# Kernel tuning notes

Measured on AMD Instinct MI355X. Metric: run time of the kernel, lower is better.

The kernel has to match this reference:

```python
import jax, jax.numpy as jnp
import numpy as np

B, S1, S2 = 8, 2048, 2048
K1D = K2D = V1D = V2D = 256
A = 128


def setup_inputs() -> dict:
    key = jax.random.key(0)
    ks = jax.random.split(key, 8)
    k1 = jax.random.normal(ks[0], (B, S1, K1D), dtype=jnp.float32)
    k2 = jax.random.normal(ks[1], (B, S2, K2D), dtype=jnp.float32)
    v1 = jax.random.normal(ks[2], (B, S1, V1D), dtype=jnp.float32)
    v2 = jax.random.normal(ks[3], (B, S2, V2D), dtype=jnp.float32)
    Wk1 = jax.random.normal(ks[4], (K1D, A), dtype=jnp.float32) / np.sqrt(K1D)
    Wk2 = jax.random.normal(ks[5], (K2D, A), dtype=jnp.float32) / np.sqrt(K2D)
    bk1 = jnp.zeros((A,), dtype=jnp.float32)
    bk2 = jnp.zeros((A,), dtype=jnp.float32)
    # lengths in [1, S-1]: avoids fully-masked softmax rows (NaN) under the XOR mask
    k1_lengths = jax.random.randint(ks[6], (B,), 1, S1, dtype=jnp.int64)
    k2_lengths = jax.random.randint(ks[7], (B,), 1, S2, dtype=jnp.int64)
    return {"k1": k1, "k2": k2, "v1": v1, "v2": v2,
            "Wk1": Wk1, "bk1": bk1, "Wk2": Wk2, "bk2": bk2,
            "k1_lengths": k1_lengths, "k2_lengths": k2_lengths}


def reference(k1, k2, v1, v2, Wk1, bk1, Wk2, bk2, k1_lengths, k2_lengths):
    b, s1, _ = k1.shape
    s2 = k2.shape[1]
    mask1 = jnp.arange(s1)[None, :] < k1_lengths[:, None]  # [B,S1] bool
    mask2 = jnp.arange(s2)[None, :] < k2_lengths[:, None]  # [B,S2] bool
    # masked where exactly one side is valid (sum == 1)
    amask = (mask1[:, :, None].astype(jnp.int32)
             + mask2[:, None, :].astype(jnp.int32)) == 1  # [B,S1,S2]
    p1 = k1 @ Wk1 + bk1  # [B,S1,A]
    p2 = k2 @ Wk2 + bk2  # [B,S2,A]
    score = jnp.einsum('bia,bja->bij', p1, p2)  # [B,S1,S2]
    score = jnp.where(amask, -jnp.inf, score)
    w1 = jax.nn.softmax(score.transpose(0, 2, 1), axis=-1)  # [B,S2,S1]
    w2 = jax.nn.softmax(score, axis=-1)                      # [B,S1,S2]
    o1 = jnp.einsum('bji,bid->bjd', w1, v1) * mask2[:, :, None].astype(v1.dtype)  # [B,S2,V1D]
    o2 = jnp.einsum('bij,bjd->bid', w2, v2) * mask1[:, :, None].astype(v2.dtype)  # [B,S1,V2D]
    return (o1, o2, w1, w2, score)
```

## Files before the change

kernel.cpp:

```cpp
#include <hip/hip_runtime.h>
#include <cstddef>

#define NB 8
#define SEQ 2048
#define KD 256
#define AD 128
#define VD 256

#define NEG_BIG (-3.0e38f)

typedef __attribute__((ext_vector_type(8))) short short8v;
typedef __attribute__((ext_vector_type(4))) float f32x4;

static __device__ __forceinline__ unsigned f2o(float f) {
    unsigned u = __float_as_uint(f);
    return (u & 0x80000000u) ? ~u : (u | 0x80000000u);
}
static __device__ __forceinline__ float o2f(unsigned o) {
    unsigned u = (o & 0x80000000u) ? (o ^ 0x80000000u) : ~o;
    return __uint_as_float(u);
}

static __device__ __forceinline__ unsigned packsplit(float w) {
    unsigned u = __float_as_uint(w);
    unsigned h = (u + 0x7fffu + ((u >> 16) & 1u)) >> 16;
    float hf = __uint_as_float(h << 16);
    unsigned u2 = __float_as_uint(w - hf);
    unsigned l = (u2 + 0x7fffu + ((u2 >> 16) & 1u)) >> 16;
    return (h << 16) | l;
}

static __device__ __forceinline__ unsigned packtrunc(float x) {
    unsigned u = __float_as_uint(x);
    unsigned hi = u & 0xffff0000u;
    float lof = x - __uint_as_float(hi);
    return hi | (__float_as_uint(lof) >> 16);
}

static __device__ __forceinline__ void unpack_frag(const unsigned* rowp, int c0,
                                                   short8v& hi, short8v& lo) {
    uint4 a = *(const uint4*)(rowp + c0);
    uint4 b = *(const uint4*)(rowp + ((c0 + 4) & 31));
    hi[0] = (short)(a.x >> 16); lo[0] = (short)(a.x);
    hi[1] = (short)(a.y >> 16); lo[1] = (short)(a.y);
    hi[2] = (short)(a.z >> 16); lo[2] = (short)(a.z);
    hi[3] = (short)(a.w >> 16); lo[3] = (short)(a.w);
    hi[4] = (short)(b.x >> 16); lo[4] = (short)(b.x);
    hi[5] = (short)(b.y >> 16); lo[5] = (short)(b.y);
    hi[6] = (short)(b.z >> 16); lo[6] = (short)(b.z);
    hi[7] = (short)(b.w >> 16); lo[7] = (short)(b.w);
}

__global__ __launch_bounds__(64) void init_kernel(
        const int* __restrict__ l1raw, const int* __restrict__ l2raw,
        int* __restrict__ lens) {
    if (threadIdx.x == 0 && blockIdx.x == 0) {
        bool i64a = (l1raw[1] == 0 && l1raw[3] == 0 && l1raw[5] == 0 && l1raw[7] == 0);
        bool i64b = (l2raw[1] == 0 && l2raw[3] == 0 && l2raw[5] == 0 && l2raw[7] == 0);
        for (int i = 0; i < NB; ++i) {
            lens[i]      = i64a ? l1raw[2 * i] : l1raw[i];
            lens[NB + i] = i64b ? l2raw[2 * i] : l2raw[i];
        }
    }
}

__global__ __launch_bounds__(256) void proj_kernel(
        const float* __restrict__ X, const float* __restrict__ W,
        const float* __restrict__ bias, float* __restrict__ P) {
    const int m0 = blockIdx.x * 64;
    const int tx = threadIdx.x % 16, ty = threadIdx.x / 16;
    __shared__ float Xs[32][68];
    __shared__ float Ws[32][132];
    float acc[4][8] = {};
    for (int k0 = 0; k0 < KD; k0 += 32) {
        {
            int t = threadIdx.x;
            int m = t >> 2;
            int fbase = (t & 3) * 2;
            const float4* src = (const float4*)(X + (size_t)(m0 + m) * KD + k0);
            #pragma unroll
            for (int q = 0; q < 2; ++q) {
                float4 v = src[fbase + q];
                int k = (fbase + q) * 4;
                Xs[k + 0][m] = v.x; Xs[k + 1][m] = v.y;
                Xs[k + 2][m] = v.z; Xs[k + 3][m] = v.w;
            }
        }
        {
            int t = threadIdx.x;
            int k = t >> 3;
            int fb = (t & 7) * 4;
            const float4* src = (const float4*)(W + (size_t)(k0 + k) * AD);
            float4* dst = (float4*)(&Ws[k][0]);
            #pragma unroll
            for (int q = 0; q < 4; ++q) dst[fb + q] = src[fb + q];
        }
        __syncthreads();
        #pragma unroll 8
        for (int kk = 0; kk < 32; ++kk) {
            float4 a = ((const float4*)(&Xs[kk][0]))[ty];
            float4 b0 = ((const float4*)(&Ws[kk][0]))[tx];
            float4 b1 = ((const float4*)(&Ws[kk][0]))[tx + 16];
            float av[4] = {a.x, a.y, a.z, a.w};
            float bv[8] = {b0.x, b0.y, b0.z, b0.w, b1.x, b1.y, b1.z, b1.w};
            #pragma unroll
            for (int i = 0; i < 4; ++i)
                #pragma unroll
                for (int j = 0; j < 8; ++j)
                    acc[i][j] = fmaf(av[i], bv[j], acc[i][j]);
        }
        __syncthreads();
    }
    float4 bias0 = ((const float4*)bias)[tx];
    float4 bias1 = ((const float4*)bias)[tx + 16];
    #pragma unroll
    for (int i = 0; i < 4; ++i) {
        int m = m0 + 4 * ty + i;
        float4 r0 = make_float4(acc[i][0] + bias0.x, acc[i][1] + bias0.y,
                                acc[i][2] + bias0.z, acc[i][3] + bias0.w);
        float4 r1 = make_float4(acc[i][4] + bias1.x, acc[i][5] + bias1.y,
                                acc[i][6] + bias1.z, acc[i][7] + bias1.w);
        float4* dst = (float4*)(P + (size_t)m * AD);
        dst[tx] = r0;
        dst[tx + 16] = r1;
    }
}

__global__ __launch_bounds__(256) void score_kernel(
        const float* __restrict__ P1, const float* __restrict__ P2,
        const int* __restrict__ lens, float* __restrict__ score,
        float* __restrict__ rp_max, float* __restrict__ rp_sum,
        float* __restrict__ cp_max, float* __restrict__ cp_sum) {
    const int b = blockIdx.z;
    const int i0 = blockIdx.y * 128, j0 = blockIdx.x * 128;
    const int tx = threadIdx.x % 16, ty = threadIdx.x / 16;
    __shared__ float As[32][132];
    __shared__ float Bs[32][132];
    __shared__ unsigned rmax_l[128], cmax_l[128];
    __shared__ float rsum_l[128], csum_l[128];
    float acc[8][8] = {};
    for (int a0 = 0; a0 < AD; a0 += 32) {
        int t = threadIdx.x;
        int r = t >> 1;
        int fb = (t & 1) * 4;
        const float4* s1 = (const float4*)(P1 + (size_t)(b * SEQ + i0 + r) * AD + a0);
        const float4* s2 = (const float4*)(P2 + (size_t)(b * SEQ + j0 + r) * AD + a0);
        #pragma unroll
        for (int q = 0; q < 4; ++q) {
            float4 v = s1[fb + q];
            float4 w = s2[fb + q];
            int k = (fb + q) * 4;
            As[k + 0][r] = v.x; As[k + 1][r] = v.y; As[k + 2][r] = v.z; As[k + 3][r] = v.w;
            Bs[k + 0][r] = w.x; Bs[k + 1][r] = w.y; Bs[k + 2][r] = w.z; Bs[k + 3][r] = w.w;
        }
        __syncthreads();
        #pragma unroll 4
        for (int kk = 0; kk < 32; ++kk) {
            const float4* Ar = (const float4*)(&As[kk][0]);
            const float4* Br = (const float4*)(&Bs[kk][0]);
            float4 a0v = Ar[ty], a1v = Ar[ty + 16];
            float4 b0v = Br[tx], b1v = Br[tx + 16];
            float av[8] = {a0v.x, a0v.y, a0v.z, a0v.w, a1v.x, a1v.y, a1v.z, a1v.w};
            float bv[8] = {b0v.x, b0v.y, b0v.z, b0v.w, b1v.x, b1v.y, b1v.z, b1v.w};
            #pragma unroll
            for (int i = 0; i < 8; ++i)
                #pragma unroll
                for (int j = 0; j < 8; ++j)
                    acc[i][j] = fmaf(av[i], bv[j], acc[i][j]);
        }
        __syncthreads();
    }
    const int len1 = lens[b], len2 = lens[NB + b];
    if (threadIdx.x < 128) {
        rmax_l[threadIdx.x] = 0u; cmax_l[threadIdx.x] = 0u; csum_l[threadIdx.x] = 0.f;
    }
    __syncthreads();
    unsigned cpart[8] = {0u, 0u, 0u, 0u, 0u, 0u, 0u, 0u};
    #pragma unroll
    for (int ii = 0; ii < 8; ++ii) {
        int il = 4 * ty + (ii & 3) + ((ii >> 2) << 6);
        int ig = i0 + il;
        bool va = ig < len1;
        unsigned rpart = 0u;
        float vals[8];
        #pragma unroll
        for (int jj = 0; jj < 8; ++jj) {
            int jl = 4 * tx + (jj & 3) + ((jj >> 2) << 6);
            int jg = j0 + jl;
            bool vb = jg < len2;
            float s = (va != vb) ? NEG_BIG : acc[ii][jj];
            vals[jj] = s;
            unsigned o = f2o(s);
            rpart = rpart > o ? rpart : o;
            cpart[jj] = cpart[jj] > o ? cpart[jj] : o;
        }
        float* dst = score + (size_t)(b * SEQ + ig) * SEQ + j0;
        ((float4*)dst)[tx]      = make_float4(vals[0], vals[1], vals[2], vals[3]);
        ((float4*)dst)[tx + 16] = make_float4(vals[4], vals[5], vals[6], vals[7]);
        atomicMax(&rmax_l[il], rpart);
    }
    #pragma unroll
    for (int jj = 0; jj < 8; ++jj) {
        int jl = 4 * tx + (jj & 3) + ((jj >> 2) << 6);
        atomicMax(&cmax_l[jl], cpart[jj]);
    }
    __syncthreads();
    float cmaxv[8];
    #pragma unroll
    for (int jj = 0; jj < 8; ++jj) {
        int jl = 4 * tx + (jj & 3) + ((jj >> 2) << 6);
        cmaxv[jj] = o2f(cmax_l[jl]);
    }
    float cs[8] = {};
    #pragma unroll
    for (int ii = 0; ii < 8; ++ii) {
        int il = 4 * ty + (ii & 3) + ((ii >> 2) << 6);
        int ig = i0 + il;
        bool va = ig < len1;
        float rmx = o2f(rmax_l[il]);
        float rs = 0.f;
        #pragma unroll
        for (int jj = 0; jj < 8; ++jj) {
            int jl = 4 * tx + (jj & 3) + ((jj >> 2) << 6);
            bool vb = (j0 + jl) < len2;
            float s = (va != vb) ? NEG_BIG : acc[ii][jj];
            rs += __expf(s - rmx);
            cs[jj] += __expf(s - cmaxv[jj]);
        }
        rs += __shfl_xor(rs, 1); rs += __shfl_xor(rs, 2);
        rs += __shfl_xor(rs, 4); rs += __shfl_xor(rs, 8);
        if (tx == 0) rsum_l[il] = rs;
    }
    #pragma unroll
    for (int jj = 0; jj < 8; ++jj) {
        float v = cs[jj];
        v += __shfl_xor(v, 16); v += __shfl_xor(v, 32);
        if (((threadIdx.x >> 4) & 3) == 0) {
            int jl = 4 * tx + (jj & 3) + ((jj >> 2) << 6);
            atomicAdd(&csum_l[jl], v);
        }
    }
    __syncthreads();
    if (threadIdx.x < 128) {
        int tt = threadIdx.x;
        size_t ri = (size_t)(b * 16 + blockIdx.x) * SEQ + i0 + tt;
        size_t ci = (size_t)(b * 16 + blockIdx.y) * SEQ + j0 + tt;
        rp_max[ri] = o2f(rmax_l[tt]);
        rp_sum[ri] = rsum_l[tt];
        cp_max[ci] = o2f(cmax_l[tt]);
        cp_sum[ci] = csum_l[tt];
    }
}

__global__ __launch_bounds__(256) void combine_kernel(
        const float* __restrict__ rp_max, const float* __restrict__ rp_sum,
        const float* __restrict__ cp_max, const float* __restrict__ cp_sum,
        float* __restrict__ rowmaxf, float* __restrict__ rowinv,
        float* __restrict__ colmaxf, float* __restrict__ colinv) {
    int gid = blockIdx.x * 256 + threadIdx.x;
    bool isCol = gid >= NB * SEQ;
    int r = isCol ? gid - NB * SEQ : gid;
    int bb = r >> 11, pos = r & (SEQ - 1);
    const float* pm = (isCol ? cp_max : rp_max) + ((size_t)(bb * 16) << 11) + pos;
    const float* ps = (isCol ? cp_sum : rp_sum) + ((size_t)(bb * 16) << 11) + pos;
    float m = pm[0];
    #pragma unroll
    for (int t = 1; t < 16; ++t) m = fmaxf(m, pm[(size_t)t << 11]);
    float s = 0.f;
    #pragma unroll
    for (int t = 0; t < 16; ++t)
        s += ps[(size_t)t << 11] * __expf(pm[(size_t)t << 11] - m);
    if (isCol) { colmaxf[r] = m; colinv[r] = 1.f / s; }
    else       { rowmaxf[r] = m; rowinv[r] = 1.f / s; }
}

__global__ __launch_bounds__(256) void o2_mfma_kernel(
        const float* __restrict__ score, const float* __restrict__ rmaxf,
        const float* __restrict__ rinvv, const float* __restrict__ V2,
        const int* __restrict__ lens, float* __restrict__ w2,
        float* __restrict__ o2) {
    const int b = blockIdx.y;
    const int m0 = blockIdx.x * 32;
    const int t = threadIdx.x;
    const int wid = t >> 6, lane = t & 63;
    const int wr = wid >> 1, wc = wid & 1;
    const int l15 = lane & 15, l4 = lane >> 4;

    __shared__ unsigned Au[32][32];
    __shared__ unsigned Bu[256][32];

    const int ia = t >> 3;
    const int jf4 = (t & 7) * 4;
    const float arm = rmaxf[b * SEQ + m0 + ia];
    const float ari = rinvv[b * SEQ + m0 + ia];
    const float* srow = score + (size_t)(b * SEQ + m0 + ia) * SEQ;
    float* wrow = w2 + (size_t)(b * SEQ + m0 + ia) * SEQ;

    const int kb = t >> 3;
    const int df = t & 7;
    const float* vbase = V2 + (size_t)(b * SEQ + kb) * VD + df * 4;

    f32x4 accM[8] = {};
    f32x4 accC[8] = {};

    float4 sc;
    float4 vv[8];
    sc = *(const float4*)(srow + jf4);
    #pragma unroll
    for (int c = 0; c < 2; ++c)
        #pragma unroll
        for (int q = 0; q < 4; ++q)
            vv[c * 4 + q] = *(const float4*)(vbase + c * 128 + q * 32);

    for (int k0 = 0; k0 < SEQ; k0 += 32) {
        float wv0 = __expf(sc.x - arm) * ari;
        float wv1 = __expf(sc.y - arm) * ari;
        float wv2 = __expf(sc.z - arm) * ari;
        float wv3 = __expf(sc.w - arm) * ari;
        uint4 pa;
        pa.x = packsplit(wv0); pa.y = packsplit(wv1);
        pa.z = packsplit(wv2); pa.w = packsplit(wv3);
        __syncthreads();
        *(uint4*)&Au[ia][(jf4 + 4 * (ia & 7)) & 31] = pa;
        #pragma unroll
        for (int c = 0; c < 2; ++c)
            #pragma unroll
            for (int q = 0; q < 4; ++q) {
                float4 v = vv[c * 4 + q];
                int d0 = c * 128 + q * 32 + df * 4;
                Bu[d0 + 0][(kb + 4 * (((d0 + 0) + ((d0 + 0) >> 4)) & 7)) & 31] = packtrunc(v.x);
                Bu[d0 + 1][(kb + 4 * (((d0 + 1) + ((d0 + 1) >> 4)) & 7)) & 31] = packtrunc(v.y);
                Bu[d0 + 2][(kb + 4 * (((d0 + 2) + ((d0 + 2) >> 4)) & 7)) & 31] = packtrunc(v.z);
                Bu[d0 + 3][(kb + 4 * (((d0 + 3) + ((d0 + 3) >> 4)) & 7)) & 31] = packtrunc(v.w);
            }
        __syncthreads();
        if (k0 + 32 < SEQ) {
            sc = *(const float4*)(srow + k0 + 32 + jf4);
            const float* vr = vbase + (size_t)(k0 + 32) * VD;
            #pragma unroll
            for (int c = 0; c < 2; ++c)
                #pragma unroll
                for (int q = 0; q < 4; ++q)
                    vv[c * 4 + q] = *(const float4*)(vr + c * 128 + q * 32);
        }
        *(float4*)(wrow + k0 + jf4) = make_float4(wv0, wv1, wv2, wv3);
        short8v ahi, alo;
        {
            int row = wr * 16 + l15;
            unpack_frag(&Au[row][0], (8 * l4 + 4 * (row & 7)) & 31, ahi, alo);
        }
        #pragma unroll
        for (int fj = 0; fj < 8; ++fj) {
            int d = wc * 128 + fj * 16 + l15;
            int c0 = (8 * l4 + 4 * ((d + (d >> 4)) & 7)) & 31;
            short8v bhi, blo;
            unpack_frag(&Bu[d][0], c0, bhi, blo);
            accM[fj] = __builtin_amdgcn_mfma_f32_16x16x32_bf16(ahi, bhi, accM[fj], 0, 0, 0);
            accC[fj] = __builtin_amdgcn_mfma_f32_16x16x32_bf16(ahi, blo, accC[fj], 0, 0, 0);
            accC[fj] = __builtin_amdgcn_mfma_f32_16x16x32_bf16(alo, bhi, accC[fj], 0, 0, 0);
        }
    }
    const int len1 = lens[b];
    #pragma unroll
    for (int r = 0; r < 4; ++r) {
        int m = m0 + wr * 16 + l4 * 4 + r;
        bool valid = m < len1;
        float* orow = o2 + (size_t)(b * SEQ + m) * VD + wc * 128 + l15;
        #pragma unroll
        for (int fj = 0; fj < 8; ++fj)
            orow[fj * 16] = valid ? (accM[fj][r] + accC[fj][r]) : 0.f;
    }
}

__global__ __launch_bounds__(256) void o1_mfma_kernel(
        const float* __restrict__ score, const float* __restrict__ cmaxf,
        const float* __restrict__ cinvv, const float* __restrict__ V1,
        const int* __restrict__ lens, float* __restrict__ w1,
        float* __restrict__ o1) {
    const int b = blockIdx.y;
    const int m0 = blockIdx.x * 32;
    const int t = threadIdx.x;
    const int wid = t >> 6, lane = t & 63;
    const int wr = wid >> 1, wc = wid & 1;
    const int l15 = lane & 15, l4 = lane >> 4;

    __shared__ unsigned Au[32][32];
    __shared__ unsigned Bu[256][32];

    const int il = t >> 3;
    const int jf4 = (t & 7) * 4;
    float4 cm = *(const float4*)(cmaxf + b * SEQ + m0 + jf4);
    float4 ci = *(const float4*)(cinvv + b * SEQ + m0 + jf4);
    const float* scol = score + (size_t)(b * SEQ + il) * SEQ + m0 + jf4;

    const int kb = t >> 3;
    const int df = t & 7;
    const float* vbase = V1 + (size_t)(b * SEQ + kb) * VD + df * 4;

    const int wj = t >> 3;
    const int wib = (t & 7) * 4;
    const int rc0 = (wib + 4 * (wj & 7)) & 31;
    float* w1row = w1 + (size_t)(b * SEQ + m0 + wj) * SEQ;

    f32x4 accM[8] = {};
    f32x4 accC[8] = {};

    float4 sc;
    float4 vv[8];
    sc = *(const float4*)(scol);
    #pragma unroll
    for (int c = 0; c < 2; ++c)
        #pragma unroll
        for (int q = 0; q < 4; ++q)
            vv[c * 4 + q] = *(const float4*)(vbase + c * 128 + q * 32);

    for (int k0 = 0; k0 < SEQ; k0 += 32) {
        float wvv[4];
        wvv[0] = __expf(sc.x - cm.x) * ci.x;
        wvv[1] = __expf(sc.y - cm.y) * ci.y;
        wvv[2] = __expf(sc.z - cm.z) * ci.z;
        wvv[3] = __expf(sc.w - cm.w) * ci.w;
        unsigned pk[4];
        #pragma unroll
        for (int e = 0; e < 4; ++e) pk[e] = packsplit(wvv[e]);
        __syncthreads();
        #pragma unroll
        for (int e = 0; e < 4; ++e)
            Au[jf4 + e][(il + 4 * ((jf4 + e) & 7)) & 31] = pk[e];
        #pragma unroll
        for (int c = 0; c < 2; ++c)
            #pragma unroll
            for (int q = 0; q < 4; ++q) {
                float4 v = vv[c * 4 + q];
                int d0 = c * 128 + q * 32 + df * 4;
                Bu[d0 + 0][(kb + 4 * (((d0 + 0) + ((d0 + 0) >> 4)) & 7)) & 31] = packtrunc(v.x);
                Bu[d0 + 1][(kb + 4 * (((d0 + 1) + ((d0 + 1) >> 4)) & 7)) & 31] = packtrunc(v.y);
                Bu[d0 + 2][(kb + 4 * (((d0 + 2) + ((d0 + 2) >> 4)) & 7)) & 31] = packtrunc(v.z);
                Bu[d0 + 3][(kb + 4 * (((d0 + 3) + ((d0 + 3) >> 4)) & 7)) & 31] = packtrunc(v.w);
            }
        __syncthreads();
        if (k0 + 32 < SEQ) {
            sc = *(const float4*)(scol + (size_t)(k0 + 32) * SEQ);
            const float* vr = vbase + (size_t)(k0 + 32) * VD;
            #pragma unroll
            for (int c = 0; c < 2; ++c)
                #pragma unroll
                for (int q = 0; q < 4; ++q)
                    vv[c * 4 + q] = *(const float4*)(vr + c * 128 + q * 32);
        }
        {
            uint4 a = *(const uint4*)(&Au[wj][rc0]);
            float f0 = __uint_as_float(a.x & 0xffff0000u) + __uint_as_float(a.x << 16);
            float f1 = __uint_as_float(a.y & 0xffff0000u) + __uint_as_float(a.y << 16);
            float f2 = __uint_as_float(a.z & 0xffff0000u) + __uint_as_float(a.z << 16);
            float f3 = __uint_as_float(a.w & 0xffff0000u) + __uint_as_float(a.w << 16);
            *(float4*)(w1row + k0 + wib) = make_float4(f0, f1, f2, f3);
        }
        short8v ahi, alo;
        {
            int row = wr * 16 + l15;
            unpack_frag(&Au[row][0], (8 * l4 + 4 * (row & 7)) & 31, ahi, alo);
        }
        #pragma unroll
        for (int fj = 0; fj < 8; ++fj) {
            int d = wc * 128 + fj * 16 + l15;
            int c0 = (8 * l4 + 4 * ((d + (d >> 4)) & 7)) & 31;
            short8v bhi, blo;
            unpack_frag(&Bu[d][0], c0, bhi, blo);
            accM[fj] = __builtin_amdgcn_mfma_f32_16x16x32_bf16(ahi, bhi, accM[fj], 0, 0, 0);
            accC[fj] = __builtin_amdgcn_mfma_f32_16x16x32_bf16(ahi, blo, accC[fj], 0, 0, 0);
            accC[fj] = __builtin_amdgcn_mfma_f32_16x16x32_bf16(alo, bhi, accC[fj], 0, 0, 0);
        }
    }
    const int len2 = lens[NB + b];
    #pragma unroll
    for (int r = 0; r < 4; ++r) {
        int m = m0 + wr * 16 + l4 * 4 + r;
        bool valid = m < len2;
        float* orow = o1 + (size_t)(b * SEQ + m) * VD + wc * 128 + l15;
        #pragma unroll
        for (int fj = 0; fj < 8; ++fj)
            orow[fj * 16] = valid ? (accM[fj][r] + accC[fj][r]) : 0.f;
    }
}

extern "C" void kernel_launch(void* const* d_in, const int* in_sizes, int n_in,
                              void* d_out, int out_size, void* d_ws, size_t ws_size,
                              hipStream_t stream) {
    const float* k1  = (const float*)d_in[0];
    const float* k2  = (const float*)d_in[1];
    const float* v1  = (const float*)d_in[2];
    const float* v2  = (const float*)d_in[3];
    const float* Wk1 = (const float*)d_in[4];
    const float* bk1 = (const float*)d_in[5];
    const float* Wk2 = (const float*)d_in[6];
    const float* bk2 = (const float*)d_in[7];
    const int* l1raw = (const int*)d_in[8];
    const int* l2raw = (const int*)d_in[9];

    float* out = (float*)d_out;
    float* o1    = out;
    float* o2    = o1 + (size_t)NB * SEQ * VD;
    float* w1    = o2 + (size_t)NB * SEQ * VD;
    float* w2    = w1 + (size_t)NB * SEQ * SEQ;
    float* score = w2 + (size_t)NB * SEQ * SEQ;

    char* ws = (char*)d_ws;
    float* p1 = (float*)ws;
    float* p2 = p1 + (size_t)NB * SEQ * AD;
    float* rowmaxf = p2 + (size_t)NB * SEQ * AD;
    float* rowinv  = rowmaxf + NB * SEQ;
    float* colmaxf = rowinv + NB * SEQ;
    float* colinv  = colmaxf + NB * SEQ;
    int* lens = (int*)(colinv + NB * SEQ);

    const size_t PTS = (size_t)NB * 16 * SEQ;
    float* rp_max = w1;
    float* rp_sum = w1 + PTS;
    float* cp_max = w1 + 2 * PTS;
    float* cp_sum = w1 + 3 * PTS;

    init_kernel<<<1, 64, 0, stream>>>(l1raw, l2raw, lens);
    proj_kernel<<<256, 256, 0, stream>>>(k1, Wk1, bk1, p1);
    proj_kernel<<<256, 256, 0, stream>>>(k2, Wk2, bk2, p2);
    score_kernel<<<dim3(16, 16, NB), 256, 0, stream>>>(p1, p2, lens, score,
                                                       rp_max, rp_sum, cp_max, cp_sum);
    combine_kernel<<<128, 256, 0, stream>>>(rp_max, rp_sum, cp_max, cp_sum,
                                            rowmaxf, rowinv, colmaxf, colinv);
    o2_mfma_kernel<<<dim3(64, NB), 256, 0, stream>>>(score, rowmaxf, rowinv,
                                                     v2, lens, w2, o2);
    o1_mfma_kernel<<<dim3(64, NB), 256, 0, stream>>>(score, colmaxf, colinv,
                                                     v1, lens, w1, o1);
}
```

Before: 841.4 us.

## Pre-pack V into split-bf16 MFMA-ready blobs and retile output per wave

New measurement: 1.337 ms. 58.9% more time.

```diff
diff --git a/kernel.cpp b/kernel.cpp
--- a/kernel.cpp
+++ b/kernel.cpp
@@ -28,13 +28,6 @@
     unsigned u2 = __float_as_uint(w - hf);
     unsigned l = (u2 + 0x7fffu + ((u2 >> 16) & 1u)) >> 16;
     return (h << 16) | l;
-}
-
-static __device__ __forceinline__ unsigned packtrunc(float x) {
-    unsigned u = __float_as_uint(x);
-    unsigned hi = u & 0xffff0000u;
-    float lof = x - __uint_as_float(hi);
-    return hi | (__float_as_uint(lof) >> 16);
 }
 
 static __device__ __forceinline__ void unpack_frag(const unsigned* rowp, int c0,
@@ -274,45 +267,66 @@
     else       { rowmaxf[r] = m; rowinv[r] = 1.f / s; }
 }
 
+__global__ __launch_bounds__(256) void vpack_kernel(
+        const float* __restrict__ V, unsigned* __restrict__ Vp) {
+    const int b = blockIdx.y, kt = blockIdx.x;
+    const int d = threadIdx.x;
+    const float* src = V + ((size_t)(b * SEQ) + kt * 32) * VD + d;
+    unsigned h[32], l[32];
+    #pragma unroll
+    for (int kk = 0; kk < 32; ++kk) {
+        float x = src[(size_t)kk * VD];
+        unsigned u = __float_as_uint(x);
+        unsigned hh = (u + 0x7fffu + ((u >> 16) & 1u)) >> 16;
+        float hf = __uint_as_float(hh << 16);
+        unsigned u2 = __float_as_uint(x - hf);
+        unsigned ll = (u2 + 0x7fffu + ((u2 >> 16) & 1u)) >> 16;
+        h[kk] = hh; l[kk] = ll;
+    }
+    unsigned* blob = Vp + (size_t)(b * 64 + kt) * 8192;
+    #pragma unroll
+    for (int c = 0; c < 4; ++c) {
+        int kbase = 8 * ((c - (d >> 1)) & 3);
+        uint4 hv, lv;
+        hv.x = h[kbase + 0] | (h[kbase + 1] << 16); hv.y = h[kbase + 2] | (h[kbase + 3] << 16);
+        hv.z = h[kbase + 4] | (h[kbase + 5] << 16); hv.w = h[kbase + 6] | (h[kbase + 7] << 16);
+        lv.x = l[kbase + 0] | (l[kbase + 1] << 16); lv.y = l[kbase + 2] | (l[kbase + 3] << 16);
+        lv.z = l[kbase + 4] | (l[kbase + 5] << 16); lv.w = l[kbase + 6] | (l[kbase + 7] << 16);
+        *(uint4*)(blob + d * 16 + c * 4)        = hv;
+        *(uint4*)(blob + 4096 + d * 16 + c * 4) = lv;
+    }
+}
+
 __global__ __launch_bounds__(256) void o2_mfma_kernel(
         const float* __restrict__ score, const float* __restrict__ rmaxf,
-        const float* __restrict__ rinvv, const float* __restrict__ V2,
+        const float* __restrict__ rinvv, const unsigned* __restrict__ Vp,
         const int* __restrict__ lens, float* __restrict__ w2,
         float* __restrict__ o2) {
     const int b = blockIdx.y;
     const int m0 = blockIdx.x * 32;
     const int t = threadIdx.x;
     const int wid = t >> 6, lane = t & 63;
-    const int wr = wid >> 1, wc = wid & 1;
     const int l15 = lane & 15, l4 = lane >> 4;
 
     __shared__ unsigned Au[32][32];
-    __shared__ unsigned Bu[256][32];
-
-    const int ia = t >> 3;
-    const int jf4 = (t & 7) * 4;
+    __shared__ __align__(16) unsigned Bs[8192];
+
+    const int ia = t >> 3, jf4 = (t & 7) * 4;
     const float arm = rmaxf[b * SEQ + m0 + ia];
     const float ari = rinvv[b * SEQ + m0 + ia];
     const float* srow = score + (size_t)(b * SEQ + m0 + ia) * SEQ;
     float* wrow = w2 + (size_t)(b * SEQ + m0 + ia) * SEQ;
 
-    const int kb = t >> 3;
-    const int df = t & 7;
-    const float* vbase = V2 + (size_t)(b * SEQ + kb) * VD + df * 4;
-
-    f32x4 accM[8] = {};
-    f32x4 accC[8] = {};
-
-    float4 sc;
-    float4 vv[8];
-    sc = *(const float4*)(srow + jf4);
-    #pragma unroll
-    for (int c = 0; c < 2; ++c)
-        #pragma unroll
-        for (int q = 0; q < 4; ++q)
-            vv[c * 4 + q] = *(const float4*)(vbase + c * 128 + q * 32);
-
-    for (int k0 = 0; k0 < SEQ; k0 += 32) {
+    const unsigned* vpb = Vp + (size_t)b * (64 * 8192) + wid * 2048 + lane * 4;
+
+    f32x4 accM[2][4] = {}, accC[2][4] = {};
+    float4 sc = *(const float4*)(srow + jf4);
+    uint4 bvv[8];
+    #pragma unroll
+    for (int i = 0; i < 8; ++i) bvv[i] = *(const uint4*)(vpb + i * 256);
+
+    for (int kt = 0; kt < 64; ++kt) {
+        const int k0 = kt * 32;
         float wv0 = __expf(sc.x - arm) * ari;
         float wv1 = __expf(sc.y - arm) * ari;
         float wv2 = __expf(sc.z - arm) * ari;
@@ -323,69 +337,63 @@
         __syncthreads();
         *(uint4*)&Au[ia][(jf4 + 4 * (ia & 7)) & 31] = pa;
         #pragma unroll
-        for (int c = 0; c < 2; ++c)
-            #pragma unroll
-            for (int q = 0; q < 4; ++q) {
-                float4 v = vv[c * 4 + q];
-                int d0 = c * 128 + q * 32 + df * 4;
-                Bu[d0 + 0][(kb + 4 * (((d0 + 0) + ((d0 + 0) >> 4)) & 7)) & 31] = packtrunc(v.x);
-                Bu[d0 + 1][(kb + 4 * (((d0 + 1) + ((d0 + 1) >> 4)) & 7)) & 31] = packtrunc(v.y);
-                Bu[d0 + 2][(kb + 4 * (((d0 + 2) + ((d0 + 2) >> 4)) & 7)) & 31] = packtrunc(v.z);
-                Bu[d0 + 3][(kb + 4 * (((d0 + 3) + ((d0 + 3) >> 4)) & 7)) & 31] = packtrunc(v.w);
+        for (int i = 0; i < 8; ++i)
+            *(uint4*)(Bs + wid * 2048 + i * 256 + lane * 4) = bvv[i];
+        *(float4*)(wrow + k0 + jf4) = make_float4(wv0, wv1, wv2, wv3);
+        __syncthreads();
+        if (kt + 1 < 64) {
+            const unsigned* ns = vpb + (size_t)(kt + 1) * 8192;
+            #pragma unroll
+            for (int i = 0; i < 8; ++i) bvv[i] = *(const uint4*)(ns + i * 256);
+            sc = *(const float4*)(srow + k0 + 32 + jf4);
+        }
+        short8v ahi[2], alo[2];
+        #pragma unroll
+        for (int fi = 0; fi < 2; ++fi) {
+            int row = fi * 16 + l15;
+            unpack_frag(&Au[row][0], (8 * l4 + 4 * (row & 7)) & 31, ahi[fi], alo[fi]);
+        }
+        #pragma unroll
+        for (int fj = 0; fj < 4; ++fj) {
+            int d = wid * 64 + fj * 16 + l15;
+            int cw = ((l4 + (d >> 1)) & 3) * 4;
+            short8v bhi = *(const short8v*)(Bs + d * 16 + cw);
+            short8v blo = *(const short8v*)(Bs + 4096 + d * 16 + cw);
+            #pragma unroll
+            for (int fi = 0; fi < 2; ++fi) {
+                accM[fi][fj] = __builtin_amdgcn_mfma_f32_16x16x32_bf16(ahi[fi], bhi, accM[fi][fj], 0, 0, 0);
+                accC[fi][fj] = __builtin_amdgcn_mfma_f32_16x16x32_bf16(ahi[fi], blo, accC[fi][fj], 0, 0, 0);
+                accC[fi][fj] = __builtin_amdgcn_mfma_f32_16x16x32_bf16(alo[fi], bhi, accC[fi][fj], 0, 0, 0);
             }
-        __syncthreads();
-        if (k0 + 32 < SEQ) {
-            sc = *(const float4*)(srow + k0 + 32 + jf4);
-            const float* vr = vbase + (size_t)(k0 + 32) * VD;
-            #pragma unroll
-            for (int c = 0; c < 2; ++c)
-                #pragma unroll
-                for (int q = 0; q < 4; ++q)
-                    vv[c * 4 + q] = *(const float4*)(vr + c * 128 + q * 32);
-        }
-        *(float4*)(wrow + k0 + jf4) = make_float4(wv0, wv1, wv2, wv3);
-        short8v ahi, alo;
-        {
-            int row = wr * 16 + l15;
-            unpack_frag(&Au[row][0], (8 * l4 + 4 * (row & 7)) & 31, ahi, alo);
-        }
-        #pragma unroll
-        for (int fj = 0; fj < 8; ++fj) {
-            int d = wc * 128 + fj * 16 + l15;
-            int c0 = (8 * l4 + 4 * ((d + (d >> 4)) & 7)) & 31;
-            short8v bhi, blo;
-            unpack_frag(&Bu[d][0], c0, bhi, blo);
-            accM[fj] = __builtin_amdgcn_mfma_f32_16x16x32_bf16(ahi, bhi, accM[fj], 0, 0, 0);
-            accC[fj] = __builtin_amdgcn_mfma_f32_16x16x32_bf16(ahi, blo, accC[fj], 0, 0, 0);
-            accC[fj] = __builtin_amdgcn_mfma_f32_16x16x32_bf16(alo, bhi, accC[fj], 0, 0, 0);
         }
     }
     const int len1 = lens[b];
     #pragma unroll
-    for (int r = 0; r < 4; ++r) {
-        int m = m0 + wr * 16 + l4 * 4 + r;
-        bool valid = m < len1;
-        float* orow = o2 + (size_t)(b * SEQ + m) * VD + wc * 128 + l15;
-        #pragma unroll
-        for (int fj = 0; fj < 8; ++fj)
-            orow[fj * 16] = valid ? (accM[fj][r] + accC[fj][r]) : 0.f;
-    }
+    for (int fi = 0; fi < 2; ++fi)
+        #pragma unroll
+        for (int r = 0; r < 4; ++r) {
+            int m = m0 + fi * 16 + l4 * 4 + r;
+            bool valid = m < len1;
+            float* orow = o2 + (size_t)(b * SEQ + m) * VD + wid * 64 + l15;
+            #pragma unroll
+            for (int fj = 0; fj < 4; ++fj)
+                orow[fj * 16] = valid ? (accM[fi][fj][r] + accC[fi][fj][r]) : 0.f;
+        }
 }
 
 __global__ __launch_bounds__(256) void o1_mfma_kernel(
         const float* __restrict__ score, const float* __restrict__ cmaxf,
-        const float* __restrict__ cinvv, const float* __restrict__ V1,
+        const float* __restrict__ cinvv, const unsigned* __restrict__ Vp,
         const int* __restrict__ lens, float* __restrict__ w1,
         float* __restrict__ o1) {
     const int b = blockIdx.y;
     const int m0 = blockIdx.x * 32;
     const int t = threadIdx.x;
     const int wid = t >> 6, lane = t & 63;
-    const int wr = wid >> 1, wc = wid & 1;
     const int l15 = lane & 15, l4 = lane >> 4;
 
     __shared__ unsigned Au[32][32];
-    __shared__ unsigned Bu[256][32];
+    __shared__ __align__(16) unsigned Bs[8192];
 
     const int il = t >> 3;
     const int jf4 = (t & 7) * 4;
@@ -393,28 +401,20 @@
     float4 ci = *(const float4*)(cinvv + b * SEQ + m0 + jf4);
     const float* scol = score + (size_t)(b * SEQ + il) * SEQ + m0 + jf4;
 
-    const int kb = t >> 3;
-    const int df = t & 7;
-    const float* vbase = V1 + (size_t)(b * SEQ + kb) * VD + df * 4;
-
-    const int wj = t >> 3;
-    const int wib = (t & 7) * 4;
+    const int wj = t >> 3, wib = (t & 7) * 4;
     const int rc0 = (wib + 4 * (wj & 7)) & 31;
     float* w1row = w1 + (size_t)(b * SEQ + m0 + wj) * SEQ;
 
-    f32x4 accM[8] = {};
-    f32x4 accC[8] = {};
-
-    float4 sc;
-    float4 vv[8];
-    sc = *(const float4*)(scol);
-    #pragma unroll
-    for (int c = 0; c < 2; ++c)
-        #pragma unroll
-        for (int q = 0; q < 4; ++q)
-            vv[c * 4 + q] = *(const float4*)(vbase + c * 128 + q * 32);
-
-    for (int k0 = 0; k0 < SEQ; k0 += 32) {
+    const unsigned* vpb = Vp + (size_t)b * (64 * 8192) + wid * 2048 + lane * 4;
+
+    f32x4 accM[2][4] = {}, accC[2][4] = {};
+    float4 sc = *(const float4*)scol;
+    uint4 bvv[8];
+    #pragma unroll
+    for (int i = 0; i < 8; ++i) bvv[i] = *(const uint4*)(vpb + i * 256);
+
+    for (int kt = 0; kt < 64; ++kt) {
+        const int k0 = kt * 32;
         float wvv[4];
         wvv[0] = __expf(sc.x - cm.x) * ci.x;
         wvv[1] = __expf(sc.y - cm.y) * ci.y;
@@ -428,25 +428,14 @@
         for (int e = 0; e < 4; ++e)
             Au[jf4 + e][(il + 4 * ((jf4 + e) & 7)) & 31] = pk[e];
         #pragma unroll
-        for (int c = 0; c < 2; ++c)
-            #pragma unroll
-            for (int q = 0; q < 4; ++q) {
-                float4 v = vv[c * 4 + q];
-                int d0 = c * 128 + q * 32 + df * 4;
-                Bu[d0 + 0][(kb + 4 * (((d0 + 0) + ((d0 + 0) >> 4)) & 7)) & 31] = packtrunc(v.x);
-                Bu[d0 + 1][(kb + 4 * (((d0 + 1) + ((d0 + 1) >> 4)) & 7)) & 31] = packtrunc(v.y);
-                Bu[d0 + 2][(kb + 4 * (((d0 + 2) + ((d0 + 2) >> 4)) & 7)) & 31] = packtrunc(v.z);
-                Bu[d0 + 3][(kb + 4 * (((d0 + 3) + ((d0 + 3) >> 4)) & 7)) & 31] = packtrunc(v.w);
-            }
-        __syncthreads();
-        if (k0 + 32 < SEQ) {
+        for (int i = 0; i < 8; ++i)
+            *(uint4*)(Bs + wid * 2048 + i * 256 + lane * 4) = bvv[i];
+        __syncthreads();
+        if (kt + 1 < 64) {
+            const unsigned* ns = vpb + (size_t)(kt + 1) * 8192;
+            #pragma unroll
+            for (int i = 0; i < 8; ++i) bvv[i] = *(const uint4*)(ns + i * 256);
             sc = *(const float4*)(scol + (size_t)(k0 + 32) * SEQ);
-            const float* vr = vbase + (size_t)(k0 + 32) * VD;
-            #pragma unroll
-            for (int c = 0; c < 2; ++c)
-                #pragma unroll
-                for (int q = 0; q < 4; ++q)
-                    vv[c * 4 + q] = *(const float4*)(vr + c * 128 + q * 32);
         }
         {
             uint4 a = *(const uint4*)(&Au[wj][rc0]);
@@ -456,32 +445,38 @@
             float f3 = __uint_as_float(a.w & 0xffff0000u) + __uint_as_float(a.w << 16);
             *(float4*)(w1row + k0 + wib) = make_float4(f0, f1, f2, f3);
         }
-        short8v ahi, alo;
-        {
-            int row = wr * 16 + l15;
-            unpack_frag(&Au[row][0], (8 * l4 + 4 * (row & 7)) & 31, ahi, alo);
-        }
-        #pragma unroll
-        for (int fj = 0; fj < 8; ++fj) {
-            int d = wc * 128 + fj * 16 + l15;
-            int c0 = (8 * l4 + 4 * ((d + (d >> 4)) & 7)) & 31;
-            short8v bhi, blo;
-            unpack_frag(&Bu[d][0], c0, bhi, blo);
-            accM[fj] = __builtin_amdgcn_mfma_f32_16x16x32_bf16(ahi, bhi, accM[fj], 0, 0, 0);
-            accC[fj] = __builtin_amdgcn_mfma_f32_16x16x32_bf16(ahi, blo, accC[fj], 0, 0, 0);
-            accC[fj] = __builtin_amdgcn_mfma_f32_16x16x32_bf16(alo, bhi, accC[fj], 0, 0, 0);
+        short8v ahi[2], alo[2];
+        #pragma unroll
+        for (int fi = 0; fi < 2; ++fi) {
+            int row = fi * 16 + l15;
+            unpack_frag(&Au[row][0], (8 * l4 + 4 * (row & 7)) & 31, ahi[fi], alo[fi]);
+        }
+        #pragma unroll
+        for (int fj = 0; fj < 4; ++fj) {
+            int d = wid * 64 + fj * 16 + l15;
+            int cw = ((l4 + (d >> 1)) & 3) * 4;
+            short8v bhi = *(const short8v*)(Bs + d * 16 + cw);
+            short8v blo = *(const short8v*)(Bs + 4096 + d * 16 + cw);
+            #pragma unroll
+            for (int fi = 0; fi < 2; ++fi) {
+                accM[fi][fj] = __builtin_amdgcn_mfma_f32_16x16x32_bf16(ahi[fi], bhi, accM[fi][fj], 0, 0, 0);
+                accC[fi][fj] = __builtin_amdgcn_mfma_f32_16x16x32_bf16(ahi[fi], blo, accC[fi][fj], 0, 0, 0);
+                accC[fi][fj] = __builtin_amdgcn_mfma_f32_16x16x32_bf16(alo[fi], bhi, accC[fi][fj], 0, 0, 0);
+            }
         }
     }
     const int len2 = lens[NB + b];
     #pragma unroll
-    for (int r = 0; r < 4; ++r) {
-        int m = m0 + wr * 16 + l4 * 4 + r;
-        bool valid = m < len2;
-        float* orow = o1 + (size_t)(b * SEQ + m) * VD + wc * 128 + l15;
-        #pragma unroll
-        for (int fj = 0; fj < 8; ++fj)
-            orow[fj * 16] = valid ? (accM[fj][r] + accC[fj][r]) : 0.f;
-    }
+    for (int fi = 0; fi < 2; ++fi)
+        #pragma unroll
+        for (int r = 0; r < 4; ++r) {
+            int m = m0 + fi * 16 + l4 * 4 + r;
+            bool valid = m < len2;
+            float* orow = o1 + (size_t)(b * SEQ + m) * VD + wid * 64 + l15;
+            #pragma unroll
+            for (int fj = 0; fj < 4; ++fj)
+                orow[fj * 16] = valid ? (accM[fi][fj][r] + accC[fi][fj][r]) : 0.f;
+        }
 }
 
 extern "C" void kernel_launch(void* const* d_in, const int* in_sizes, int n_in,
@@ -514,6 +509,8 @@
     float* colinv  = colmaxf + NB * SEQ;
     int* lens = (int*)(colinv + NB * SEQ);
 
+    unsigned* Vpw = (unsigned*)ws;
+
     const size_t PTS = (size_t)NB * 16 * SEQ;
     float* rp_max = w1;
     float* rp_sum = w1 + PTS;
@@ -527,8 +524,10 @@
                                                        rp_max, rp_sum, cp_max, cp_sum);
     combine_kernel<<<128, 256, 0, stream>>>(rp_max, rp_sum, cp_max, cp_sum,
                                             rowmaxf, rowinv, colmaxf, colinv);
+    vpack_kernel<<<dim3(64, NB), 256, 0, stream>>>(v2, Vpw);
     o2_mfma_kernel<<<dim3(64, NB), 256, 0, stream>>>(score, rowmaxf, rowinv,
-                                                     v2, lens, w2, o2);
+                                                     Vpw, lens, w2, o2);
+    vpack_kernel<<<dim3(64, NB), 256, 0, stream>>>(v1, Vpw);
     o1_mfma_kernel<<<dim3(64, NB), 256, 0, stream>>>(score, colmaxf, colinv,
-                                                     v1, lens, w1, o1);
-}
+                                                     Vpw, lens, w1, o1);
+}
```
